# Optimization experiments

Hardware: AMD Instinct MI355X
Metric: run time of the kernel (lower is better)

The kernel has to match this reference:

```python
import jax, jax.numpy as jnp
from jax import lax
import numpy as np

T, N, E = 4, 50000, 1600000
IN_CH, HID, OUT = 128, 128, 16


def setup_inputs() -> dict:
    key = jax.random.key(0)
    ks = jax.random.split(key, 10)
    s = lambda fan: 1.0 / np.sqrt(fan)
    return {
        "xs": jax.random.normal(ks[0], (T, N, IN_CH), jnp.float32),
        "edges": jax.random.randint(ks[1], (T, 2, E), 0, N, dtype=jnp.int32),
        "W_gcn": jax.random.normal(ks[2], (HID, IN_CH), jnp.float32) * s(IN_CH),
        "b_gcn": jax.random.normal(ks[3], (HID,), jnp.float32) * s(IN_CH),
        "W_ih": jax.random.normal(ks[4], (3 * HID, HID), jnp.float32) * s(HID),
        "W_hh": jax.random.normal(ks[5], (3 * HID, HID), jnp.float32) * s(HID),
        "b_ih": jax.random.normal(ks[6], (3 * HID,), jnp.float32) * s(HID),
        "b_hh": jax.random.normal(ks[7], (3 * HID,), jnp.float32) * s(HID),
        "W_cls": jax.random.normal(ks[8], (OUT, HID), jnp.float32) * s(HID),
        "b_cls": jax.random.normal(ks[9], (OUT,), jnp.float32) * s(HID),
    }


def reference(xs, edges, W_gcn, b_gcn, W_ih, W_hh, b_ih, b_hh, W_cls, b_cls):
    n = xs.shape[1]
    loop = jnp.arange(n, dtype=edges.dtype)

    def gcn_forward(x, ei):
        src = jnp.concatenate([ei[0], loop])  # add self loops
        dst = jnp.concatenate([ei[1], loop])
        h = x @ W_gcn.T + b_gcn                               # [N, H]
        agg = jax.ops.segment_sum(h[src], dst, num_segments=n)  # scatter_add features
        deg = jax.ops.segment_sum(jnp.ones(dst.shape[0], h.dtype), dst, num_segments=n)
        return jax.nn.relu(agg / jnp.maximum(deg, 1.0)[:, None])

    def gru_cell(z, h):
        gi = z @ W_ih.T + b_ih   # [1, 3H]
        gh = h @ W_hh.T + b_hh
        ir, iz, ig = jnp.split(gi, 3, axis=1)
        hr, hz, hg = jnp.split(gh, 3, axis=1)
        r = jax.nn.sigmoid(ir + hr)
        zg = jax.nn.sigmoid(iz + hz)
        ng = jnp.tanh(ig + r * hg)
        return (1.0 - zg) * ng + zg * h

    def step(h, snap):
        x, ei = snap
        z_mean = gcn_forward(x, ei).mean(axis=0, keepdims=True)  # [1, H]
        return gru_cell(z_mean, h), None

    h0 = jnp.zeros((1, W_hh.shape[1]), xs.dtype)
    h, _ = lax.scan(step, h0, (xs, edges))
    return h @ W_cls.T + b_cls  # [1, OUT]
```

## Files before the change

kernel.cpp:

```cpp
#include <hip/hip_runtime.h>
#include <hip/hip_bf16.h>

typedef unsigned int u32;
typedef unsigned short u16;
typedef unsigned char u8;
typedef __attribute__((ext_vector_type(8))) __bf16 bfrag;
typedef __attribute__((ext_vector_type(4))) float f32x4;
typedef __attribute__((ext_vector_type(2))) float f32x2;

#define T_STEPS 4
#define N_NODES 50000
#define E_EDGES 1600000
#define HID 128
#define OUT_CH 16

#define NCHUNK 128
#define CHUNK (E_EDGES / NCHUNK)
#define NBKT 196
#define BCAP 10240

#define H_STRIDE    6400000u
#define HALF_STRIDE 3200000u
#define RS_STRIDE   204800u
#define ZP_STRIDE   16384u
#define CSR_STRIDE  3200000u

#define OFF_H     0u
#define OFF_RS    25600000u
#define OFF_ZPAD  26419200u
#define OFF_CSR   26484736u
#define OFF_WB    39284736u
#define OFF_GCNT  39317504u
#define OFF_RECS  39321600u

__device__ __forceinline__ u8 f32_to_fp8(float v) {
    return (u8)(__builtin_amdgcn_cvt_pk_fp8_f32(v, v, 0, 0) & 0xFF);
}

__global__ void wbf_kernel(const float* __restrict__ W, __bf16* __restrict__ wb) {
    const int i = blockIdx.x * 256 + threadIdx.x;
    wb[i] = (__bf16)W[i];
}

__global__ __launch_bounds__(256) void gemm_mfma_kernel(const float* __restrict__ xs,
                                                        const __bf16* __restrict__ wb,
                                                        const float* __restrict__ b,
                                                        u8* __restrict__ h8_all) {
    const int lane = threadIdx.x & 63;
    const int wv   = threadIdx.x >> 6;
    const int r16  = lane & 15;
    const int quad = lane >> 4;
    const int mb   = blockIdx.x;
    const int t    = blockIdx.y;
    const float* x = xs + (size_t)t * N_NODES * 128;
    u8* h8         = h8_all + (size_t)t * H_STRIDE;

    bfrag Bf[2][4];
#pragma unroll
    for (int nt = 0; nt < 2; ++nt) {
        const int c = wv * 32 + nt * 16 + r16;
#pragma unroll
        for (int ks = 0; ks < 4; ++ks)
            Bf[nt][ks] = *(const bfrag*)(wb + c * 128 + ks * 32 + quad * 8);
    }

    const float* xp = x + (size_t)(mb * 16 + r16) * 128 + quad * 8;
    bfrag Af[4];
#pragma unroll
    for (int ks = 0; ks < 4; ++ks) {
        const float4 v0 = *(const float4*)(xp + ks * 32);
        const float4 v1 = *(const float4*)(xp + ks * 32 + 4);
        Af[ks][0] = (__bf16)v0.x; Af[ks][1] = (__bf16)v0.y;
        Af[ks][2] = (__bf16)v0.z; Af[ks][3] = (__bf16)v0.w;
        Af[ks][4] = (__bf16)v1.x; Af[ks][5] = (__bf16)v1.y;
        Af[ks][6] = (__bf16)v1.z; Af[ks][7] = (__bf16)v1.w;
    }

    f32x4 acc0 = {0.f, 0.f, 0.f, 0.f};
    f32x4 acc1 = {0.f, 0.f, 0.f, 0.f};
#pragma unroll
    for (int ks = 0; ks < 4; ++ks) {
        acc0 = __builtin_amdgcn_mfma_f32_16x16x32_bf16(Af[ks], Bf[0][ks], acc0, 0, 0, 0);
        acc1 = __builtin_amdgcn_mfma_f32_16x16x32_bf16(Af[ks], Bf[1][ks], acc1, 0, 0, 0);
    }

    const int c0   = wv * 32 + r16;
    const int half = wv >> 1;
    const int col0 = c0 - half * 64;
    u8* hb = h8 + half * HALF_STRIDE;
    const float b0 = b[c0], b1 = b[c0 + 16];
#pragma unroll
    for (int r = 0; r < 4; ++r) {
        const size_t row = (size_t)(mb * 16 + quad * 4 + r) * 64;
        hb[row + col0]      = f32_to_fp8(acc0[r] + b0);
        hb[row + col0 + 16] = f32_to_fp8(acc1[r] + b1);
    }
}

__global__ __launch_bounds__(256) void part_kernel(const int* __restrict__ edges,
                                                   u32* __restrict__ gcnt,
                                                   u32* __restrict__ recs) {
    __shared__ u32 bh[NBKT], bc[NBKT];
    const int id  = blockIdx.x;
    const int xcd = id & 7;
    const int t   = xcd >> 1;
    const int c   = ((xcd & 1) << 6) | (id >> 3);
    const int base = c * CHUNK;
    const int* src = edges + (size_t)t * 2 * E_EDGES;
    const int* dst = src + E_EDGES;
    u32* rt = recs + (size_t)t * NBKT * BCAP;
    const int tid = threadIdx.x;

    if (tid < NBKT) bh[tid] = 0;
    __syncthreads();
    for (int i = tid; i < CHUNK; i += 256)
        atomicAdd(&bh[dst[base + i] >> 8], 1u);
    __syncthreads();
    if (tid < NBKT) bc[tid] = atomicAdd(&gcnt[t * 256 + tid], bh[tid]);
    __syncthreads();
    for (int i = tid; i < CHUNK; i += 256) {
        const int d = dst[base + i];
        const int s = src[base + i];
        const int bkt = d >> 8;
        const u32 idx = atomicAdd(&bc[bkt], 1u);
        if (idx < (u32)BCAP)
            rt[(size_t)bkt * BCAP + idx] = ((u32)(d & 255) << 16) | (u32)s;
    }
}

__global__ __launch_bounds__(256) void build_kernel(const u32* __restrict__ recs,
                                                    const u32* __restrict__ gcnt,
                                                    int* __restrict__ rs_all,
                                                    u16* __restrict__ csr_all) {
    __shared__ u32 ncnt[256];
    __shared__ u32 ncur[256];
    __shared__ u32 sc[256];
    __shared__ u16 cl[BCAP];
    const int id  = blockIdx.x;
    const int xcd = id & 7;
    const int t   = xcd >> 1;
    const int b   = ((xcd & 1) ? 98 : 0) + (id >> 3);
    const int tid = threadIdx.x;
    const u32 cnt = min(gcnt[t * 256 + b], (u32)BCAP);
    const u32* rp = recs + ((size_t)t * NBKT + b) * BCAP;
    int* rs  = rs_all + (size_t)t * (RS_STRIDE / 4);
    u16* csr = csr_all + (size_t)t * (CSR_STRIDE / 2);

    sc[tid] = (tid < NBKT) ? min(gcnt[t * 256 + tid], (u32)BCAP) : 0u;
    __syncthreads();
    for (int d = 1; d < 256; d <<= 1) {
        const u32 v = (tid >= d) ? sc[tid - d] : 0u;
        __syncthreads();
        sc[tid] += v;
        __syncthreads();
    }
    const u32 rbase = sc[b] - cnt;

    ncnt[tid] = 0;
    __syncthreads();
    for (u32 i = tid; i < cnt; i += 256)
        atomicAdd(&ncnt[rp[i] >> 16], 1u);
    __syncthreads();
    const u32 mine = ncnt[tid];
    for (int d = 1; d < 256; d <<= 1) {
        const u32 v = (tid >= d) ? ncnt[tid - d] : 0u;
        __syncthreads();
        ncnt[tid] += v;
        __syncthreads();
    }
    const u32 off = ncnt[tid] - mine;
    ncur[tid] = off;
    const int n = b * 256 + tid;
    if (n <= N_NODES) rs[n] = (int)(rbase + off);
    __syncthreads();
    for (u32 i = tid; i < cnt; i += 256) {
        const u32 r = rp[i];
        const u32 p = atomicAdd(&ncur[r >> 16], 1u);
        cl[p] = (u16)(r & 0xFFFFu);
    }
    __syncthreads();
    for (u32 i = tid; i < cnt; i += 256)
        csr[rbase + i] = cl[i];
}

__global__ __launch_bounds__(256) void gather_kernel(const u32* __restrict__ h8_all,
                                                     const int* __restrict__ rs_all,
                                                     const u16* __restrict__ csr_all,
                                                     float* __restrict__ zp_all) {
    const int lane = threadIdx.x & 63;
    const int wv   = __builtin_amdgcn_readfirstlane((int)(threadIdx.x >> 6));
    const int qh   = lane & 15;
    const int quar = lane >> 4;
    const int id   = blockIdx.x;
    const int xcd  = id & 7;
    const int t    = xcd >> 1;
    const int half = xcd & 1;
    const int kb   = id >> 3;
    const u32* h8d = h8_all + (size_t)t * (H_STRIDE / 4) + half * (HALF_STRIDE / 4);
    const int* row_start = rs_all + (size_t)t * (RS_STRIDE / 4);
    const u16* csr = csr_all + (size_t)t * (CSR_STRIDE / 2);
    float* z_pad = zp_all + (size_t)t * (ZP_STRIDE / 4);
    const int gw   = kb * 4 + wv;
    const int nw   = 1024 * 4;

    float z0 = 0.f, z1 = 0.f, z2 = 0.f, z3 = 0.f;
    for (int n = gw; n < N_NODES; n += nw) {
        const int rs  = row_start[n];
        const int cnt = row_start[n + 1] - rs;
        const u32 us = h8d[n * 16 + qh];
        const bool q0 = (quar == 0);
        f32x2 acc01 = q0 ? __builtin_amdgcn_cvt_pk_f32_fp8(us, 0) : (f32x2){0.f, 0.f};
        f32x2 acc23 = q0 ? __builtin_amdgcn_cvt_pk_f32_fp8(us, 1) : (f32x2){0.f, 0.f};

        const u16* lst = csr + rs;
        int i = 0;
        for (; i + 32 <= cnt; i += 32) {
            int s[8];
            u32 u[8];
#pragma unroll
            for (int k = 0; k < 8; ++k) s[k] = lst[i + k * 4 + quar];
#pragma unroll
            for (int k = 0; k < 8; ++k) u[k] = h8d[s[k] * 16 + qh];
#pragma unroll
            for (int k = 0; k < 8; ++k) {
                acc01 = acc01 + __builtin_amdgcn_cvt_pk_f32_fp8(u[k], 0);
                acc23 = acc23 + __builtin_amdgcn_cvt_pk_f32_fp8(u[k], 1);
            }
        }
        for (; i < cnt; i += 16) {
            int s[4];
            u32 u[4];
            bool v[4];
#pragma unroll
            for (int k = 0; k < 4; ++k) {
                const int idx = i + k * 4 + quar;
                v[k] = idx < cnt;
                s[k] = lst[v[k] ? idx : 0];
            }
#pragma unroll
            for (int k = 0; k < 4; ++k) u[k] = v[k] ? h8d[s[k] * 16 + qh] : 0u;
#pragma unroll
            for (int k = 0; k < 4; ++k) {
                acc01 = acc01 + __builtin_amdgcn_cvt_pk_f32_fp8(u[k], 0);
                acc23 = acc23 + __builtin_amdgcn_cvt_pk_f32_fp8(u[k], 1);
            }
        }
        float a0 = acc01.x, a1 = acc01.y, a2 = acc23.x, a3 = acc23.y;
        a0 += __shfl_xor(a0, 16); a0 += __shfl_xor(a0, 32);
        a1 += __shfl_xor(a1, 16); a1 += __shfl_xor(a1, 32);
        a2 += __shfl_xor(a2, 16); a2 += __shfl_xor(a2, 32);
        a3 += __shfl_xor(a3, 16); a3 += __shfl_xor(a3, 32);
        const float inv = 1.0f / (float)(cnt + 1);
        z0 += fmaxf(a0 * inv, 0.f);
        z1 += fmaxf(a1 * inv, 0.f);
        z2 += fmaxf(a2 * inv, 0.f);
        z3 += fmaxf(a3 * inv, 0.f);
    }

    __shared__ float red[4][16][4];
    if (lane < 16) {
        red[wv][lane][0] = z0;
        red[wv][lane][1] = z1;
        red[wv][lane][2] = z2;
        red[wv][lane][3] = z3;
    }
    __syncthreads();
    if (threadIdx.x < 64) {
        const int c = threadIdx.x;
        const int g = c >> 2, m = c & 3;
        float s = 0.f;
#pragma unroll
        for (int w = 0; w < 4; ++w) s += red[w][g][m];
        atomicAdd(&z_pad[(half * 64 + c) * 32], s);
    }
}

__global__ __launch_bounds__(512) void gru_all_kernel(const float* __restrict__ zp_all,
                                                      const float* __restrict__ W_ih,
                                                      const float* __restrict__ W_hh,
                                                      const float* __restrict__ b_ih,
                                                      const float* __restrict__ b_hh,
                                                      const float* __restrict__ W_cls,
                                                      const float* __restrict__ b_cls,
                                                      float* __restrict__ out) {
    __shared__ float zm[128], hs[128], gi[384], gh[384];
    const int tid = threadIdx.x;
    if (tid < 128) hs[tid] = 0.f;
    for (int t = 0; t < T_STEPS; ++t) {
        if (tid < 128)
            zm[tid] = zp_all[(size_t)t * (ZP_STRIDE / 4) + tid * 32] * (1.0f / (float)N_NODES);
        __syncthreads();
        if (tid < 384) {
            float a = b_ih[tid], g = b_hh[tid];
            const float* wi = W_ih + tid * 128;
            const float* wh = W_hh + tid * 128;
#pragma unroll 8
            for (int k = 0; k < 128; ++k) {
                a = fmaf(zm[k], wi[k], a);
                g = fmaf(hs[k], wh[k], g);
            }
            gi[tid] = a;
            gh[tid] = g;
        }
        __syncthreads();
        if (tid < 128) {
            const float r  = 1.f / (1.f + expf(-(gi[tid] + gh[tid])));
            const float zg = 1.f / (1.f + expf(-(gi[128 + tid] + gh[128 + tid])));
            const float ng = tanhf(gi[256 + tid] + r * gh[256 + tid]);
            hs[tid] = (1.f - zg) * ng + zg * hs[tid];
        }
        __syncthreads();
    }
    if (tid < OUT_CH) {
        float a = b_cls[tid];
        const float* wc = W_cls + tid * 128;
#pragma unroll 8
        for (int k = 0; k < 128; ++k) a = fmaf(hs[k], wc[k], a);
        out[tid] = a;
    }
}

extern "C" void kernel_launch(void* const* d_in, const int* in_sizes, int n_in,
                              void* d_out, int out_size, void* d_ws, size_t ws_size,
                              hipStream_t stream) {
    const float* xs    = (const float*)d_in[0];
    const int*   edges = (const int*)d_in[1];
    const float* W_gcn = (const float*)d_in[2];
    const float* b_gcn = (const float*)d_in[3];
    const float* W_ih  = (const float*)d_in[4];
    const float* W_hh  = (const float*)d_in[5];
    const float* b_ih  = (const float*)d_in[6];
    const float* b_hh  = (const float*)d_in[7];
    const float* W_cls = (const float*)d_in[8];
    const float* b_cls = (const float*)d_in[9];
    float* out = (float*)d_out;

    char* ws = (char*)d_ws;
    u8*    h8        = (u8*)(ws + OFF_H);
    int*   row_start = (int*)(ws + OFF_RS);
    float* z_pad     = (float*)(ws + OFF_ZPAD);
    u16*   csr       = (u16*)(ws + OFF_CSR);
    __bf16* wb       = (__bf16*)(ws + OFF_WB);
    u32*   gcnt      = (u32*)(ws + OFF_GCNT);
    u32*   recs      = (u32*)(ws + OFF_RECS);

    hipMemsetAsync(z_pad, 0, 4 * ZP_STRIDE, stream);
    hipMemsetAsync(gcnt, 0, 4096, stream);
    wbf_kernel<<<64, 256, 0, stream>>>(W_gcn, wb);

    gemm_mfma_kernel<<<dim3(3125, T_STEPS), 256, 0, stream>>>(xs, wb, b_gcn, h8);
    part_kernel<<<NCHUNK * T_STEPS, 256, 0, stream>>>(edges, gcnt, recs);
    build_kernel<<<98 * 8, 256, 0, stream>>>(recs, gcnt, row_start, csr);
    gather_kernel<<<2048 * T_STEPS, 256, 0, stream>>>((const u32*)h8, row_start, csr, z_pad);
    gru_all_kernel<<<1, 512, 0, stream>>>(z_pad, W_ih, W_hh, b_ih, b_hh,
                                          W_cls, b_cls, out);
}
```

Before: 553.2 us.

## Stage partitioned edges in LDS for coalesced bucket writes; split gather launch

```diff
diff --git a/kernel.cpp b/kernel.cpp
--- a/kernel.cpp
+++ b/kernel.cpp
@@ -100,7 +100,12 @@
 __global__ __launch_bounds__(256) void part_kernel(const int* __restrict__ edges,
                                                    u32* __restrict__ gcnt,
                                                    u32* __restrict__ recs) {
-    __shared__ u32 bh[NBKT], bc[NBKT];
+    __shared__ u32 bh[NBKT];
+    __shared__ u32 sc[256];
+    __shared__ u32 lob[NBKT];
+    __shared__ u32 cur[NBKT];
+    __shared__ u32 gof[NBKT];
+    __shared__ u32 staged[CHUNK];
     const int id  = blockIdx.x;
     const int xcd = id & 7;
     const int t   = xcd >> 1;
@@ -116,15 +121,38 @@
     for (int i = tid; i < CHUNK; i += 256)
         atomicAdd(&bh[dst[base + i] >> 8], 1u);
     __syncthreads();
-    if (tid < NBKT) bc[tid] = atomicAdd(&gcnt[t * 256 + tid], bh[tid]);
+    sc[tid] = (tid < NBKT) ? bh[tid] : 0u;
+    __syncthreads();
+    for (int d = 1; d < 256; d <<= 1) {
+        const u32 v = (tid >= d) ? sc[tid - d] : 0u;
+        __syncthreads();
+        sc[tid] += v;
+        __syncthreads();
+    }
+    if (tid < NBKT) {
+        const u32 lo = sc[tid] - bh[tid];
+        lob[tid] = lo;
+        cur[tid] = lo;
+        gof[tid] = atomicAdd(&gcnt[t * 256 + tid], bh[tid]);
+    }
     __syncthreads();
     for (int i = tid; i < CHUNK; i += 256) {
         const int d = dst[base + i];
         const int s = src[base + i];
-        const int bkt = d >> 8;
-        const u32 idx = atomicAdd(&bc[bkt], 1u);
-        if (idx < (u32)BCAP)
-            rt[(size_t)bkt * BCAP + idx] = ((u32)(d & 255) << 16) | (u32)s;
+        const u32 p = atomicAdd(&cur[d >> 8], 1u);
+        staged[p] = ((u32)(d & 255) << 16) | (u32)s;
+    }
+    __syncthreads();
+    for (int i = tid; i < CHUNK; i += 256) {
+        int b = 0;
+#pragma unroll
+        for (int s = 128; s > 0; s >>= 1) {
+            const int cand = b + s;
+            if (cand < NBKT && lob[cand] <= (u32)i) b = cand;
+        }
+        const u32 gp = gof[b] + ((u32)i - lob[b]);
+        if (gp < (u32)BCAP)
+            rt[(size_t)b * BCAP + gp] = staged[i];
     }
 }
 
@@ -186,7 +214,8 @@
 __global__ __launch_bounds__(256) void gather_kernel(const u32* __restrict__ h8_all,
                                                      const int* __restrict__ rs_all,
                                                      const u16* __restrict__ csr_all,
-                                                     float* __restrict__ zp_all) {
+                                                     float* __restrict__ zp_all,
+                                                     int nbase) {
     const int lane = threadIdx.x & 63;
     const int wv   = __builtin_amdgcn_readfirstlane((int)(threadIdx.x >> 6));
     const int qh   = lane & 15;
@@ -201,10 +230,11 @@
     const u16* csr = csr_all + (size_t)t * (CSR_STRIDE / 2);
     float* z_pad = zp_all + (size_t)t * (ZP_STRIDE / 4);
     const int gw   = kb * 4 + wv;
-    const int nw   = 1024 * 4;
+    const int nw   = 512 * 4;
+    const int nend = nbase + N_NODES / 2;
 
     float z0 = 0.f, z1 = 0.f, z2 = 0.f, z3 = 0.f;
-    for (int n = gw; n < N_NODES; n += nw) {
+    for (int n = nbase + gw; n < nend; n += nw) {
         const int rs  = row_start[n];
         const int cnt = row_start[n + 1] - rs;
         const u32 us = h8d[n * 16 + qh];
@@ -351,7 +381,8 @@
     gemm_mfma_kernel<<<dim3(3125, T_STEPS), 256, 0, stream>>>(xs, wb, b_gcn, h8);
     part_kernel<<<NCHUNK * T_STEPS, 256, 0, stream>>>(edges, gcnt, recs);
     build_kernel<<<98 * 8, 256, 0, stream>>>(recs, gcnt, row_start, csr);
-    gather_kernel<<<2048 * T_STEPS, 256, 0, stream>>>((const u32*)h8, row_start, csr, z_pad);
+    gather_kernel<<<4096, 256, 0, stream>>>((const u32*)h8, row_start, csr, z_pad, 0);
+    gather_kernel<<<4096, 256, 0, stream>>>((const u32*)h8, row_start, csr, z_pad, N_NODES / 2);
     gru_all_kernel<<<1, 512, 0, stream>>>(z_pad, W_ih, W_hh, b_ih, b_hh,
                                           W_cls, b_cls, out);
 }
```

Measured after the change: 538.7 us. 1.03x faster.
